# Performance work log

Hardware: AMD Instinct MI355X
Metric: run time of the kernel (lower is better)

Reference implementation:

```python
import jax, jax.numpy as jnp
import numpy as np

B, S, D = 4, 2048, 1024


def setup_inputs() -> dict:
    key = jax.random.key(0)
    kx, kq, kk, kv, km = jax.random.split(key, 5)
    x = jax.random.normal(kx, (B, S, D), dtype=jnp.float32)
    # bias-free Linear weights, torch convention W: (out, in), y = x @ W.T
    Wq = jax.random.normal(kq, (D, D), dtype=jnp.float32) * 0.02
    Wk = jax.random.normal(kk, (D, D), dtype=jnp.float32) * 0.02
    Wv = jax.random.normal(kv, (D, D), dtype=jnp.float32) * 0.02
    # quantum mask: probability vector per batch over seq positions
    q_mask = jax.nn.softmax(jax.random.normal(km, (B, S), dtype=jnp.float32), axis=-1)
    return {"x": x, "Wq": Wq, "Wk": Wk, "Wv": Wv, "q_mask": q_mask}


def reference(x, Wq, Wk, Wv, q_mask):
    # projections (torch Linear: x @ W.T)
    q = jnp.einsum("bsd,ed->bse", x, Wq)
    k = jnp.einsum("bsd,ed->bse", x, Wk)
    v = jnp.einsum("bsd,ed->bse", x, Wv)
    scale = 1.0 / jnp.sqrt(jnp.asarray(D, dtype=x.dtype))
    scores = jnp.einsum("bqe,bke->bqk", q, k) * scale  # (B, S, S)
    # per-row multiplicative quantum mask (mask broadcast over key dim)
    scores = scores * q_mask[:, :, None]
    attn = jax.nn.softmax(scores, axis=-1)
    out = jnp.einsum("bqk,bkd->bqd", attn, v)
    return out
```

## Files before the change

kernel.cpp:

```cpp
#include <hip/hip_runtime.h>
#include <hip/hip_bf16.h>

#define BB 4
#define SS 2048
#define DD 1024

using f32x4  = __attribute__((ext_vector_type(4))) float;
using i32x4  = __attribute__((ext_vector_type(4))) int;
using i32x8  = __attribute__((ext_vector_type(8))) int;

struct f8_t { unsigned char b; };

__device__ __forceinline__ void gld16(const void* g, void* l) {
    __builtin_amdgcn_global_load_lds(
        (const __attribute__((address_space(1))) void*)(g),
        (__attribute__((address_space(3))) void*)(l),
        16, 0, 0);
}

__device__ __forceinline__ void store1(float* p, float v) { *p = v; }
__device__ __forceinline__ void store1(f8_t* p, float v)  {
    p->b = (unsigned char)(__builtin_amdgcn_cvt_pk_fp8_f32(v, v, 0, false) & 0xff);
}

__global__ void cvt_x_kernel(const float* __restrict__ x, unsigned char* __restrict__ x8, int n8) {
    int i = blockIdx.x * blockDim.x + threadIdx.x;
    if (i >= n8) return;
    float4 a = ((const float4*)x)[2 * i];
    float4 b = ((const float4*)x)[2 * i + 1];
    int lo = __builtin_amdgcn_cvt_pk_fp8_f32(a.x, a.y, 0, false);
    lo     = __builtin_amdgcn_cvt_pk_fp8_f32(a.z, a.w, lo, true);
    int hi = __builtin_amdgcn_cvt_pk_fp8_f32(b.x, b.y, 0, false);
    hi     = __builtin_amdgcn_cvt_pk_fp8_f32(b.z, b.w, hi, true);
    ((int2*)x8)[i] = make_int2(lo, hi);
}

__global__ void cvt_w_kernel(const float* __restrict__ Wq, const float* __restrict__ Wk,
                             const float* __restrict__ Wv, unsigned char* __restrict__ w8, int n8) {
    int i = blockIdx.x * blockDim.x + threadIdx.x;
    int seg = i / n8;
    int j = i - seg * n8;
    const float* src = (seg == 0) ? Wq : (seg == 1) ? Wk : Wv;
    float4 a = ((const float4*)src)[2 * j];
    float4 b = ((const float4*)src)[2 * j + 1];
    int lo = __builtin_amdgcn_cvt_pk_fp8_f32(a.x, a.y, 0, false);
    lo     = __builtin_amdgcn_cvt_pk_fp8_f32(a.z, a.w, lo, true);
    int hi = __builtin_amdgcn_cvt_pk_fp8_f32(b.x, b.y, 0, false);
    hi     = __builtin_amdgcn_cvt_pk_fp8_f32(b.z, b.w, hi, true);
    ((int2*)(w8 + (size_t)seg * n8 * 8))[j] = make_int2(lo, hi);
}

__global__ void xsum_kernel(const float* __restrict__ x, float* __restrict__ xsum) {
    int bd = blockIdx.x;
    int b  = bd >> 2, dc = bd & 3;
    int d  = dc * 256 + threadIdx.x;
    int s0 = blockIdx.y * 128;
    const float* p = x + ((size_t)b * SS + s0) * DD + d;
    float acc = 0.f;
    for (int i = 0; i < 128; ++i) acc += p[(size_t)i * DD];
    atomicAdd(&xsum[b * DD + d], acc);
}

__global__ void colsumv_kernel(const float* __restrict__ Wv, const float* __restrict__ xsum,
                               float* __restrict__ colsum) {
    int idx  = blockIdx.x * 4 + (threadIdx.x >> 6);
    int b    = idx >> 10, c = idx & 1023;
    int lane = threadIdx.x & 63;
    const float* wr = Wv + (size_t)c * DD;
    const float* xs = xsum + b * DD;
    float acc = 0.f;
#pragma unroll 4
    for (int d = lane; d < DD; d += 64) acc += wr[d] * xs[d];
#pragma unroll
    for (int off = 32; off; off >>= 1) acc += __shfl_xor(acc, off);
    if (lane == 0) colsum[idx] = acc;
}

template <int MODE, typename CT>
__global__ __launch_bounds__(256, 3) void gemm_f8(
    const unsigned char* __restrict__ A, const unsigned char* __restrict__ B,
    CT* __restrict__ C, int M, int N, int K,
    long batchA, long batchB, long batchC,
    int ldc, int col_shift, long cstride,
    const float* __restrict__ qmask, float* __restrict__ rsum,
    const float* __restrict__ colsum) {
    constexpr int BM = 128, BN = 128, BK = 128;
    constexpr int SCALE_A = (MODE == 3) ? 118 : 127;
    __shared__ __attribute__((aligned(16))) unsigned char As[BM * BK];
    __shared__ __attribute__((aligned(16))) unsigned char Bs[BN * BK];

    const int tid  = threadIdx.x;
    const int lane = tid & 63;
    const int wv   = tid >> 6;
    const int l16  = lane & 15;
    const int quad = lane >> 4;
    const int wm   = wv >> 1;
    const int wn   = wv & 1;

    const int m0 = blockIdx.y * BM;
    const int n0 = blockIdx.x * BN;
    const long z = blockIdx.z;
    const unsigned char* Ab = A + z * batchA;
    const unsigned char* Bb = B + z * batchB;

    const int sA = (2 * quad) ^ (l16 & 7);

    f32x4 acc[4][4] = {};

    for (int kt = 0; kt < K; kt += BK) {
#pragma unroll
        for (int j = 0; j < 4; ++j) {
            int slot = j * 256 + wv * 64 + lane;
            int r = slot >> 3;
            int c = (slot & 7) ^ (r & 7);
            gld16(Ab + (size_t)(m0 + r) * K + (kt + c * 16),
                  As + (size_t)(j * 256 + wv * 64) * 16);
        }
#pragma unroll
        for (int j = 0; j < 4; ++j) {
            int slot = j * 256 + wv * 64 + lane;
            int r = slot >> 3;
            int c = (slot & 7) ^ (r & 7);
            gld16(Bb + (size_t)(n0 + r) * K + (kt + c * 16),
                  Bs + (size_t)(j * 256 + wv * 64) * 16);
        }
        asm volatile("s_waitcnt vmcnt(0)" ::: "memory");
        __syncthreads();

        i32x8 af[4], bfr[4];
#pragma unroll
        for (int i = 0; i < 4; ++i) {
            int r = wm * 64 + i * 16 + l16;
            i32x4 p0 = *(const i32x4*)(As + r * 128 + sA * 16);
            i32x4 p1 = *(const i32x4*)(As + r * 128 + (sA ^ 1) * 16);
            af[i][0]=p0[0]; af[i][1]=p0[1]; af[i][2]=p0[2]; af[i][3]=p0[3];
            af[i][4]=p1[0]; af[i][5]=p1[1]; af[i][6]=p1[2]; af[i][7]=p1[3];
        }
#pragma unroll
        for (int i = 0; i < 4; ++i) {
            int r = wn * 64 + i * 16 + l16;
            i32x4 p0 = *(const i32x4*)(Bs + r * 128 + sA * 16);
            i32x4 p1 = *(const i32x4*)(Bs + r * 128 + (sA ^ 1) * 16);
            bfr[i][0]=p0[0]; bfr[i][1]=p0[1]; bfr[i][2]=p0[2]; bfr[i][3]=p0[3];
            bfr[i][4]=p1[0]; bfr[i][5]=p1[1]; bfr[i][6]=p1[2]; bfr[i][7]=p1[3];
        }

#pragma unroll
        for (int i = 0; i < 4; ++i)
#pragma unroll
            for (int j = 0; j < 4; ++j)
                acc[i][j] = __builtin_amdgcn_mfma_scale_f32_16x16x128_f8f6f4(
                    af[i], bfr[j], acc[i][j], 0, 0, 0, SCALE_A, 0, 127);
        __syncthreads();
    }

    CT* Cb = C + z * batchC;

    if constexpr (MODE == 0) {
#pragma unroll
        for (int mi = 0; mi < 4; ++mi)
#pragma unroll
            for (int ni = 0; ni < 4; ++ni) {
                int colg = n0 + wn * 64 + ni * 16 + l16;
#pragma unroll
                for (int r = 0; r < 4; ++r) {
                    int rowg = m0 + wm * 64 + mi * 16 + quad * 4 + r;
                    store1(Cb + (size_t)rowg * ldc + colg, acc[mi][ni][r]);
                }
            }
    } else if constexpr (MODE == 1) {
#pragma unroll
        for (int mi = 0; mi < 4; ++mi)
#pragma unroll
            for (int ni = 0; ni < 4; ++ni) {
                int colg = n0 + wn * 64 + ni * 16 + l16;
                int cb   = colg >> col_shift;
                int ccol = colg - (cb << col_shift);
#pragma unroll
                for (int r = 0; r < 4; ++r) {
                    int rowg = m0 + wm * 64 + mi * 16 + quad * 4 + r;
                    store1(Cb + (long)cb * cstride + (size_t)rowg * ldc + ccol, acc[mi][ni][r]);
                }
            }
    } else if constexpr (MODE == 2) {
        const float* qm = qmask + (z << 11);
        float* rs = rsum + (z << 11);
#pragma unroll
        for (int mi = 0; mi < 4; ++mi) {
#pragma unroll
            for (int r = 0; r < 4; ++r) {
                int rowg = m0 + wm * 64 + mi * 16 + quad * 4 + r;
                float fac = qm[rowg] * 0.03125f;
                float part = 0.f;
#pragma unroll
                for (int ni = 0; ni < 4; ++ni) {
                    int colg = n0 + wn * 64 + ni * 16 + l16;
                    float t = __expf(acc[mi][ni][r] * fac) - 1.0f;
                    part += t;
                    store1(Cb + (size_t)rowg * ldc + colg, t * 512.0f);
                }
                part += __shfl_xor(part, 1);
                part += __shfl_xor(part, 2);
                part += __shfl_xor(part, 4);
                part += __shfl_xor(part, 8);
                if (l16 == 0) atomicAdd(&rs[rowg], part);
            }
        }
    } else {
        const float* rs = rsum + (z << 11);
        const float* cs = colsum + (z << 10);
#pragma unroll
        for (int mi = 0; mi < 4; ++mi) {
#pragma unroll
            for (int r = 0; r < 4; ++r) {
                int rowg = m0 + wm * 64 + mi * 16 + quad * 4 + r;
                float inv = 1.0f / (2048.0f + rs[rowg]);
#pragma unroll
                for (int ni = 0; ni < 4; ++ni) {
                    int colg = n0 + wn * 64 + ni * 16 + l16;
                    store1(Cb + (size_t)rowg * ldc + colg, (acc[mi][ni][r] + cs[colg]) * inv);
                }
            }
        }
    }
}

extern "C" void kernel_launch(void* const* d_in, const int* in_sizes, int n_in,
                              void* d_out, int out_size, void* d_ws, size_t ws_size,
                              hipStream_t stream) {
    const float* x     = (const float*)d_in[0];
    const float* Wq    = (const float*)d_in[1];
    const float* Wk    = (const float*)d_in[2];
    const float* Wv    = (const float*)d_in[3];
    const float* qmask = (const float*)d_in[4];
    float* out = (float*)d_out;

    const long nx = (long)BB * SS * DD;
    const long nw = (long)DD * DD;

    unsigned char* ws  = (unsigned char*)d_ws;
    unsigned char* x8  = ws;
    unsigned char* w8  = x8 + nx;
    unsigned char* qk8 = w8 + 3 * nw;
    unsigned char* vt8 = qk8 + 2 * nx;
    unsigned char* t8  = vt8 + nx;
    float* xsum   = (float*)(t8 + (long)BB * SS * SS);
    float* rs     = xsum + BB * DD;
    float* colsum = rs + BB * SS;

    hipMemsetAsync(xsum, 0, (size_t)(BB * DD + BB * SS) * sizeof(float), stream);

    cvt_x_kernel<<<dim3((int)(nx / 8 / 256)), dim3(256), 0, stream>>>(x, x8, (int)(nx / 8));
    cvt_w_kernel<<<dim3((int)(3 * nw / 8 / 256)), dim3(256), 0, stream>>>(Wq, Wk, Wv, w8, (int)(nw / 8));
    xsum_kernel<<<dim3(16, 16), dim3(256), 0, stream>>>(x, xsum);
    colsumv_kernel<<<dim3(1024), dim3(256), 0, stream>>>(Wv, xsum, colsum);

    gemm_f8<0, f8_t><<<dim3(DD / 128, (BB * SS) / 128, 2), 256, 0, stream>>>(
        x8, w8, (f8_t*)qk8, BB * SS, DD, DD, 0, nw, nx, DD, 31, 0, nullptr, nullptr, nullptr);

    gemm_f8<1, f8_t><<<dim3((BB * SS) / 128, DD / 128, 1), 256, 0, stream>>>(
        w8 + 2 * nw, x8, (f8_t*)vt8, DD, BB * SS, DD, 0, 0, 0, SS, 11, (long)DD * SS,
        nullptr, nullptr, nullptr);

    gemm_f8<2, f8_t><<<dim3(SS / 128, SS / 128, BB), 256, 0, stream>>>(
        qk8, qk8 + nx, (f8_t*)t8, SS, SS, DD, (long)SS * DD, (long)SS * DD, (long)SS * SS,
        SS, 31, 0, qmask, rs, nullptr);

    gemm_f8<3, float><<<dim3(DD / 128, SS / 128, BB), 256, 0, stream>>>(
        t8, vt8, out, SS, DD, SS, (long)SS * SS, (long)DD * SS, (long)SS * DD,
        DD, 31, 0, nullptr, rs, colsum);
}
```

Before: 207.5 us.

## Double-buffer LDS in fp8 GEMM with 256x128 tiles and interleaved MFMA phases

The fp8 GEMM tile grows to 256x128 with 512 threads (8 waves), and the K loop is rebuilt around double-buffered LDS. The next tile's global-to-LDS loads are issued in chunks between the MFMA phases, and s_setprio raises wave priority during the MFMA bursts. The goal is to hide global load latency behind compute and to reuse each B tile across more rows. In exchange the kernel uses more LDS (96KB), adds more barriers per iteration and runs fewer blocks per CU, which may lower occupancy. The epilogue indexing (wm/wn with 8 waves) must still match the new tile shape.

```diff
diff --git a/kernel.cpp b/kernel.cpp
--- a/kernel.cpp
+++ b/kernel.cpp
@@ -77,17 +77,17 @@
 }
 
 template <int MODE, typename CT>
-__global__ __launch_bounds__(256, 3) void gemm_f8(
+__global__ __launch_bounds__(512, 2) void gemm_f8(
     const unsigned char* __restrict__ A, const unsigned char* __restrict__ B,
     CT* __restrict__ C, int M, int N, int K,
     long batchA, long batchB, long batchC,
     int ldc, int col_shift, long cstride,
     const float* __restrict__ qmask, float* __restrict__ rsum,
     const float* __restrict__ colsum) {
-    constexpr int BM = 128, BN = 128, BK = 128;
+    constexpr int BM = 256, BN = 128, BK = 128;
     constexpr int SCALE_A = (MODE == 3) ? 118 : 127;
-    __shared__ __attribute__((aligned(16))) unsigned char As[BM * BK];
-    __shared__ __attribute__((aligned(16))) unsigned char Bs[BN * BK];
+    __shared__ __attribute__((aligned(16))) unsigned char As[2][BM * BK];
+    __shared__ __attribute__((aligned(16))) unsigned char Bs[2][BN * BK];
 
     const int tid  = threadIdx.x;
     const int lane = tid & 63;
@@ -103,56 +103,94 @@
     const unsigned char* Ab = A + z * batchA;
     const unsigned char* Bb = B + z * batchB;
 
-    const int sA = (2 * quad) ^ (l16 & 7);
+    const int cbase = 2 * quad;
 
     f32x4 acc[4][4] = {};
 
-    for (int kt = 0; kt < K; kt += BK) {
-#pragma unroll
-        for (int j = 0; j < 4; ++j) {
-            int slot = j * 256 + wv * 64 + lane;
-            int r = slot >> 3;
-            int c = (slot & 7) ^ (r & 7);
-            gld16(Ab + (size_t)(m0 + r) * K + (kt + c * 16),
-                  As + (size_t)(j * 256 + wv * 64) * 16);
-        }
-#pragma unroll
-        for (int j = 0; j < 4; ++j) {
-            int slot = j * 256 + wv * 64 + lane;
-            int r = slot >> 3;
-            int c = (slot & 7) ^ (r & 7);
-            gld16(Bb + (size_t)(n0 + r) * K + (kt + c * 16),
-                  Bs + (size_t)(j * 256 + wv * 64) * 16);
-        }
+#define STAGE_A(buf, kt, j) do {                                              \
+        int slot_ = (j) * 512 + tid;                                          \
+        int r_ = slot_ >> 3;                                                  \
+        int c_ = (slot_ & 7) ^ (r_ & 7);                                      \
+        gld16(Ab + (size_t)(m0 + r_) * K + ((kt) + c_ * 16),                  \
+              &As[buf][((j) * 512 + wv * 64) * 16]);                          \
+    } while (0)
+#define STAGE_B(buf, kt, j) do {                                              \
+        int slot_ = (j) * 512 + tid;                                          \
+        int r_ = slot_ >> 3;                                                  \
+        int c_ = (slot_ & 7) ^ (r_ & 7);                                      \
+        gld16(Bb + (size_t)(n0 + r_) * K + ((kt) + c_ * 16),                  \
+              &Bs[buf][((j) * 512 + wv * 64) * 16]);                          \
+    } while (0)
+#define RDFRAG(f, base, r) do {                                               \
+        int cc_ = cbase ^ ((r) & 7);                                          \
+        i32x4 p0_ = *(const i32x4*)((base) + (r) * 128 + cc_ * 16);           \
+        i32x4 p1_ = *(const i32x4*)((base) + (r) * 128 + (cc_ ^ 1) * 16);     \
+        f[0]=p0_[0]; f[1]=p0_[1]; f[2]=p0_[2]; f[3]=p0_[3];                   \
+        f[4]=p1_[0]; f[5]=p1_[1]; f[6]=p1_[2]; f[7]=p1_[3];                   \
+    } while (0)
+#define MFMA(d, a, b) \
+        d = __builtin_amdgcn_mfma_scale_f32_16x16x128_f8f6f4(a, b, d, 0, 0, 0, SCALE_A, 0, 127)
+
+    STAGE_A(0, 0, 0); STAGE_A(0, 0, 1); STAGE_A(0, 0, 2); STAGE_A(0, 0, 3);
+    STAGE_B(0, 0, 0); STAGE_B(0, 0, 1);
+    asm volatile("s_waitcnt vmcnt(0)" ::: "memory");
+    __builtin_amdgcn_s_barrier();
+
+    const int NT = K / BK;
+    for (int t = 0; t < NT; ++t) {
+        const int cur = t & 1;
+        const int nxt = cur ^ 1;
+        const unsigned char* Ac = &As[cur][0];
+        const unsigned char* Bc = &Bs[cur][0];
+        const int ktn = (t + 1) * BK;
+        const bool pf = (t + 1 < NT);
+
+        i32x8 a0, a1, a2, a3, b0, b1, b2, b3;
+
+        RDFRAG(a0, Ac, wm * 64 +  0 + l16);
+        RDFRAG(a1, Ac, wm * 64 + 16 + l16);
+        RDFRAG(b0, Bc, wn * 64 +  0 + l16);
+        RDFRAG(b1, Bc, wn * 64 + 16 + l16);
+        if (pf) { STAGE_A(nxt, ktn, 0); STAGE_A(nxt, ktn, 1); STAGE_A(nxt, ktn, 2); }
+        __builtin_amdgcn_s_barrier();
+        asm volatile("s_waitcnt lgkmcnt(0)" ::: "memory");
+        __builtin_amdgcn_sched_barrier(0);
+        __builtin_amdgcn_s_setprio(1);
+        MFMA(acc[0][0], a0, b0); MFMA(acc[0][1], a0, b1);
+        MFMA(acc[1][0], a1, b0); MFMA(acc[1][1], a1, b1);
+        __builtin_amdgcn_s_setprio(0);
+        __builtin_amdgcn_s_barrier();
+
+        RDFRAG(b2, Bc, wn * 64 + 32 + l16);
+        RDFRAG(b3, Bc, wn * 64 + 48 + l16);
+        if (pf) { STAGE_A(nxt, ktn, 3); STAGE_B(nxt, ktn, 0); STAGE_B(nxt, ktn, 1); }
+        __builtin_amdgcn_s_barrier();
+        asm volatile("s_waitcnt lgkmcnt(0)" ::: "memory");
+        __builtin_amdgcn_sched_barrier(0);
+        __builtin_amdgcn_s_setprio(1);
+        MFMA(acc[0][2], a0, b2); MFMA(acc[0][3], a0, b3);
+        MFMA(acc[1][2], a1, b2); MFMA(acc[1][3], a1, b3);
+        __builtin_amdgcn_s_setprio(0);
+        __builtin_amdgcn_s_barrier();
+
+        RDFRAG(a2, Ac, wm * 64 + 32 + l16);
+        RDFRAG(a3, Ac, wm * 64 + 48 + l16);
+        __builtin_amdgcn_s_barrier();
+        asm volatile("s_waitcnt lgkmcnt(0)" ::: "memory");
+        __builtin_amdgcn_sched_barrier(0);
+        __builtin_amdgcn_s_setprio(1);
+        MFMA(acc[2][2], a2, b2); MFMA(acc[2][3], a2, b3);
+        MFMA(acc[3][2], a3, b2); MFMA(acc[3][3], a3, b3);
+        MFMA(acc[2][0], a2, b0); MFMA(acc[2][1], a2, b1);
+        MFMA(acc[3][0], a3, b0); MFMA(acc[3][1], a3, b1);
+        __builtin_amdgcn_s_setprio(0);
         asm volatile("s_waitcnt vmcnt(0)" ::: "memory");
-        __syncthreads();
-
-        i32x8 af[4], bfr[4];
-#pragma unroll
-        for (int i = 0; i < 4; ++i) {
-            int r = wm * 64 + i * 16 + l16;
-            i32x4 p0 = *(const i32x4*)(As + r * 128 + sA * 16);
-            i32x4 p1 = *(const i32x4*)(As + r * 128 + (sA ^ 1) * 16);
-            af[i][0]=p0[0]; af[i][1]=p0[1]; af[i][2]=p0[2]; af[i][3]=p0[3];
-            af[i][4]=p1[0]; af[i][5]=p1[1]; af[i][6]=p1[2]; af[i][7]=p1[3];
-        }
-#pragma unroll
-        for (int i = 0; i < 4; ++i) {
-            int r = wn * 64 + i * 16 + l16;
-            i32x4 p0 = *(const i32x4*)(Bs + r * 128 + sA * 16);
-            i32x4 p1 = *(const i32x4*)(Bs + r * 128 + (sA ^ 1) * 16);
-            bfr[i][0]=p0[0]; bfr[i][1]=p0[1]; bfr[i][2]=p0[2]; bfr[i][3]=p0[3];
-            bfr[i][4]=p1[0]; bfr[i][5]=p1[1]; bfr[i][6]=p1[2]; bfr[i][7]=p1[3];
-        }
-
-#pragma unroll
-        for (int i = 0; i < 4; ++i)
-#pragma unroll
-            for (int j = 0; j < 4; ++j)
-                acc[i][j] = __builtin_amdgcn_mfma_scale_f32_16x16x128_f8f6f4(
-                    af[i], bfr[j], acc[i][j], 0, 0, 0, SCALE_A, 0, 127);
-        __syncthreads();
+        __builtin_amdgcn_s_barrier();
     }
+#undef STAGE_A
+#undef STAGE_B
+#undef RDFRAG
+#undef MFMA
 
     CT* Cb = C + z * batchC;
 
@@ -255,18 +293,18 @@
     xsum_kernel<<<dim3(16, 16), dim3(256), 0, stream>>>(x, xsum);
     colsumv_kernel<<<dim3(1024), dim3(256), 0, stream>>>(Wv, xsum, colsum);
 
-    gemm_f8<0, f8_t><<<dim3(DD / 128, (BB * SS) / 128, 2), 256, 0, stream>>>(
+    gemm_f8<0, f8_t><<<dim3(DD / 128, (BB * SS) / 256, 2), 512, 0, stream>>>(
         x8, w8, (f8_t*)qk8, BB * SS, DD, DD, 0, nw, nx, DD, 31, 0, nullptr, nullptr, nullptr);
 
-    gemm_f8<1, f8_t><<<dim3((BB * SS) / 128, DD / 128, 1), 256, 0, stream>>>(
+    gemm_f8<1, f8_t><<<dim3((BB * SS) / 128, DD / 256, 1), 512, 0, stream>>>(
         w8 + 2 * nw, x8, (f8_t*)vt8, DD, BB * SS, DD, 0, 0, 0, SS, 11, (long)DD * SS,
         nullptr, nullptr, nullptr);
 
-    gemm_f8<2, f8_t><<<dim3(SS / 128, SS / 128, BB), 256, 0, stream>>>(
+    gemm_f8<2, f8_t><<<dim3(SS / 128, SS / 256, BB), 512, 0, stream>>>(
         qk8, qk8 + nx, (f8_t*)t8, SS, SS, DD, (long)SS * DD, (long)SS * DD, (long)SS * SS,
         SS, 31, 0, qmask, rs, nullptr);
 
-    gemm_f8<3, float><<<dim3(DD / 128, SS / 128, BB), 256, 0, stream>>>(
+    gemm_f8<3, float><<<dim3(DD / 128, SS / 256, BB), 512, 0, stream>>>(
         t8, vt8, out, SS, DD, SS, (long)SS * SS, (long)DD * SS, (long)SS * DD,
         DD, 31, 0, nullptr, rs, colsum);
 }
```

New measurement: 230.2 us. 10.9% more time.

## Switch FP8 GEMM to 32x32x64 MFMA tiles and raise occupancy bound

Applied to the files above, without the earlier changes.

Replaces the 16x16x128 scaled FP8 MFMA with the 32x32x64 variant, so each wave computes a 2x2 grid of 32x32 tiles over two K sub-steps instead of a 4x4 grid of 16x16 tiles. This cuts the number of LDS fragment reads per MFMA output and the MFMA issue count, and all epilogues are remapped to the 32x32 accumulator layout. Launch bounds rise from 3 to 4 blocks per CU to encourage more occupancy, which tightens the register budget and could cause spills.

```diff
diff --git a/kernel.cpp b/kernel.cpp
--- a/kernel.cpp
+++ b/kernel.cpp
@@ -6,6 +6,7 @@
 #define DD 1024
 
 using f32x4  = __attribute__((ext_vector_type(4))) float;
+using f32x16 = __attribute__((ext_vector_type(16))) float;
 using i32x4  = __attribute__((ext_vector_type(4))) int;
 using i32x8  = __attribute__((ext_vector_type(8))) int;
 
@@ -77,7 +78,7 @@
 }
 
 template <int MODE, typename CT>
-__global__ __launch_bounds__(256, 3) void gemm_f8(
+__global__ __launch_bounds__(256, 4) void gemm_f8(
     const unsigned char* __restrict__ A, const unsigned char* __restrict__ B,
     CT* __restrict__ C, int M, int N, int K,
     long batchA, long batchB, long batchC,
@@ -92,8 +93,9 @@
     const int tid  = threadIdx.x;
     const int lane = tid & 63;
     const int wv   = tid >> 6;
-    const int l16  = lane & 15;
-    const int quad = lane >> 4;
+    const int l31  = lane & 31;
+    const int half = lane >> 5;
+    const int hb   = half * 2;
     const int wm   = wv >> 1;
     const int wn   = wv & 1;
 
@@ -103,99 +105,93 @@
     const unsigned char* Ab = A + z * batchA;
     const unsigned char* Bb = B + z * batchB;
 
-    const int sA = (2 * quad) ^ (l16 & 7);
-
-    f32x4 acc[4][4] = {};
+    f32x16 acc[2][2] = {};
+
+#define STAGE(dst, src, kt, j) do {                                           \
+        int slot_ = (j) * 256 + tid;                                          \
+        int r_ = slot_ >> 3;                                                  \
+        int c_ = (slot_ & 7) ^ (r_ & 7);                                      \
+        gld16((src) + (size_t)r_ * K + ((kt) + c_ * 16),                      \
+              (dst) + (size_t)((j) * 256 + wv * 64) * 16);                    \
+    } while (0)
+#define RDFRAG(f, base, rr, s) do {                                           \
+        int r_ = (rr);                                                        \
+        int c0_ = (s) * 4 + hb;                                               \
+        const unsigned char* rp_ = (base) + r_ * 128;                         \
+        i32x4 q0_ = *(const i32x4*)(rp_ + ((c0_ ^ (r_ & 7)) * 16));           \
+        i32x4 q1_ = *(const i32x4*)(rp_ + (((c0_ + 1) ^ (r_ & 7)) * 16));     \
+        f[0]=q0_[0]; f[1]=q0_[1]; f[2]=q0_[2]; f[3]=q0_[3];                   \
+        f[4]=q1_[0]; f[5]=q1_[1]; f[6]=q1_[2]; f[7]=q1_[3];                   \
+    } while (0)
+#define MFMA(d, a, b) \
+        d = __builtin_amdgcn_mfma_scale_f32_32x32x64_f8f6f4(a, b, d, 0, 0, 0, SCALE_A, 0, 127)
 
     for (int kt = 0; kt < K; kt += BK) {
-#pragma unroll
-        for (int j = 0; j < 4; ++j) {
-            int slot = j * 256 + wv * 64 + lane;
-            int r = slot >> 3;
-            int c = (slot & 7) ^ (r & 7);
-            gld16(Ab + (size_t)(m0 + r) * K + (kt + c * 16),
-                  As + (size_t)(j * 256 + wv * 64) * 16);
-        }
-#pragma unroll
-        for (int j = 0; j < 4; ++j) {
-            int slot = j * 256 + wv * 64 + lane;
-            int r = slot >> 3;
-            int c = (slot & 7) ^ (r & 7);
-            gld16(Bb + (size_t)(n0 + r) * K + (kt + c * 16),
-                  Bs + (size_t)(j * 256 + wv * 64) * 16);
-        }
+        STAGE(As, Ab + (size_t)m0 * K, kt, 0); STAGE(As, Ab + (size_t)m0 * K, kt, 1);
+        STAGE(As, Ab + (size_t)m0 * K, kt, 2); STAGE(As, Ab + (size_t)m0 * K, kt, 3);
+        STAGE(Bs, Bb + (size_t)n0 * K, kt, 0); STAGE(Bs, Bb + (size_t)n0 * K, kt, 1);
+        STAGE(Bs, Bb + (size_t)n0 * K, kt, 2); STAGE(Bs, Bb + (size_t)n0 * K, kt, 3);
         asm volatile("s_waitcnt vmcnt(0)" ::: "memory");
         __syncthreads();
 
-        i32x8 af[4], bfr[4];
-#pragma unroll
-        for (int i = 0; i < 4; ++i) {
-            int r = wm * 64 + i * 16 + l16;
-            i32x4 p0 = *(const i32x4*)(As + r * 128 + sA * 16);
-            i32x4 p1 = *(const i32x4*)(As + r * 128 + (sA ^ 1) * 16);
-            af[i][0]=p0[0]; af[i][1]=p0[1]; af[i][2]=p0[2]; af[i][3]=p0[3];
-            af[i][4]=p1[0]; af[i][5]=p1[1]; af[i][6]=p1[2]; af[i][7]=p1[3];
+#pragma unroll
+        for (int s = 0; s < 2; ++s) {
+            i32x8 a0, a1, b0, b1;
+            RDFRAG(a0, As, wm * 64 +  0 + l31, s);
+            RDFRAG(a1, As, wm * 64 + 32 + l31, s);
+            RDFRAG(b0, Bs, wn * 64 +  0 + l31, s);
+            RDFRAG(b1, Bs, wn * 64 + 32 + l31, s);
+            MFMA(acc[0][0], a0, b0); MFMA(acc[0][1], a0, b1);
+            MFMA(acc[1][0], a1, b0); MFMA(acc[1][1], a1, b1);
         }
-#pragma unroll
-        for (int i = 0; i < 4; ++i) {
-            int r = wn * 64 + i * 16 + l16;
-            i32x4 p0 = *(const i32x4*)(Bs + r * 128 + sA * 16);
-            i32x4 p1 = *(const i32x4*)(Bs + r * 128 + (sA ^ 1) * 16);
-            bfr[i][0]=p0[0]; bfr[i][1]=p0[1]; bfr[i][2]=p0[2]; bfr[i][3]=p0[3];
-            bfr[i][4]=p1[0]; bfr[i][5]=p1[1]; bfr[i][6]=p1[2]; bfr[i][7]=p1[3];
-        }
-
-#pragma unroll
-        for (int i = 0; i < 4; ++i)
-#pragma unroll
-            for (int j = 0; j < 4; ++j)
-                acc[i][j] = __builtin_amdgcn_mfma_scale_f32_16x16x128_f8f6f4(
-                    af[i], bfr[j], acc[i][j], 0, 0, 0, SCALE_A, 0, 127);
         __syncthreads();
     }
+#undef STAGE
+#undef RDFRAG
+#undef MFMA
 
     CT* Cb = C + z * batchC;
 
     if constexpr (MODE == 0) {
 #pragma unroll
-        for (int mi = 0; mi < 4; ++mi)
-#pragma unroll
-            for (int ni = 0; ni < 4; ++ni) {
-                int colg = n0 + wn * 64 + ni * 16 + l16;
-#pragma unroll
-                for (int r = 0; r < 4; ++r) {
-                    int rowg = m0 + wm * 64 + mi * 16 + quad * 4 + r;
-                    store1(Cb + (size_t)rowg * ldc + colg, acc[mi][ni][r]);
+        for (int mi = 0; mi < 2; ++mi)
+#pragma unroll
+            for (int ni = 0; ni < 2; ++ni) {
+                int colg = n0 + wn * 64 + ni * 32 + l31;
+#pragma unroll
+                for (int reg = 0; reg < 16; ++reg) {
+                    int rowg = m0 + wm * 64 + mi * 32 + (reg & 3) + 8 * (reg >> 2) + 4 * half;
+                    store1(Cb + (size_t)rowg * ldc + colg, acc[mi][ni][reg]);
                 }
             }
     } else if constexpr (MODE == 1) {
 #pragma unroll
-        for (int mi = 0; mi < 4; ++mi)
-#pragma unroll
-            for (int ni = 0; ni < 4; ++ni) {
-                int colg = n0 + wn * 64 + ni * 16 + l16;
+        for (int mi = 0; mi < 2; ++mi)
+#pragma unroll
+            for (int ni = 0; ni < 2; ++ni) {
+                int colg = n0 + wn * 64 + ni * 32 + l31;
                 int cb   = colg >> col_shift;
                 int ccol = colg - (cb << col_shift);
 #pragma unroll
-                for (int r = 0; r < 4; ++r) {
-                    int rowg = m0 + wm * 64 + mi * 16 + quad * 4 + r;
-                    store1(Cb + (long)cb * cstride + (size_t)rowg * ldc + ccol, acc[mi][ni][r]);
+                for (int reg = 0; reg < 16; ++reg) {
+                    int rowg = m0 + wm * 64 + mi * 32 + (reg & 3) + 8 * (reg >> 2) + 4 * half;
+                    store1(Cb + (long)cb * cstride + (size_t)rowg * ldc + ccol, acc[mi][ni][reg]);
                 }
             }
     } else if constexpr (MODE == 2) {
         const float* qm = qmask + (z << 11);
         float* rs = rsum + (z << 11);
 #pragma unroll
-        for (int mi = 0; mi < 4; ++mi) {
-#pragma unroll
-            for (int r = 0; r < 4; ++r) {
-                int rowg = m0 + wm * 64 + mi * 16 + quad * 4 + r;
+        for (int mi = 0; mi < 2; ++mi) {
+#pragma unroll
+            for (int reg = 0; reg < 16; ++reg) {
+                int rowg = m0 + wm * 64 + mi * 32 + (reg & 3) + 8 * (reg >> 2) + 4 * half;
                 float fac = qm[rowg] * 0.03125f;
                 float part = 0.f;
 #pragma unroll
-                for (int ni = 0; ni < 4; ++ni) {
-                    int colg = n0 + wn * 64 + ni * 16 + l16;
-                    float t = __expf(acc[mi][ni][r] * fac) - 1.0f;
+                for (int ni = 0; ni < 2; ++ni) {
+                    int colg = n0 + wn * 64 + ni * 32 + l31;
+                    float t = __expf(acc[mi][ni][reg] * fac) - 1.0f;
                     part += t;
                     store1(Cb + (size_t)rowg * ldc + colg, t * 512.0f);
                 }
@@ -203,22 +199,23 @@
                 part += __shfl_xor(part, 2);
                 part += __shfl_xor(part, 4);
                 part += __shfl_xor(part, 8);
-                if (l16 == 0) atomicAdd(&rs[rowg], part);
+                part += __shfl_xor(part, 16);
+                if (l31 == 0) atomicAdd(&rs[rowg], part);
             }
         }
     } else {
         const float* rs = rsum + (z << 11);
         const float* cs = colsum + (z << 10);
 #pragma unroll
-        for (int mi = 0; mi < 4; ++mi) {
-#pragma unroll
-            for (int r = 0; r < 4; ++r) {
-                int rowg = m0 + wm * 64 + mi * 16 + quad * 4 + r;
+        for (int mi = 0; mi < 2; ++mi) {
+#pragma unroll
+            for (int reg = 0; reg < 16; ++reg) {
+                int rowg = m0 + wm * 64 + mi * 32 + (reg & 3) + 8 * (reg >> 2) + 4 * half;
                 float inv = 1.0f / (2048.0f + rs[rowg]);
 #pragma unroll
-                for (int ni = 0; ni < 4; ++ni) {
-                    int colg = n0 + wn * 64 + ni * 16 + l16;
-                    store1(Cb + (size_t)rowg * ldc + colg, (acc[mi][ni][r] + cs[colg]) * inv);
+                for (int ni = 0; ni < 2; ++ni) {
+                    int colg = n0 + wn * 64 + ni * 32 + l31;
+                    store1(Cb + (size_t)rowg * ldc + colg, (acc[mi][ni][reg] + cs[colg]) * inv);
                 }
             }
         }
```

After: 214.5 us. 3.4% more time.
